# Optimization experiments

Hardware: AMD Instinct MI355X
Metric: run time of the kernel (lower is better)

The kernel has to match this reference:

```python
import jax, jax.numpy as jnp
import numpy as np

LDDT_THRESHOLDS = jnp.array([0.5, 1.0, 2.0, 4.0], dtype=jnp.float32)
NUCLEIC_ACID_CUTOFF = 30.0
OTHER_CUTOFF = 15.0


def _cdist(x):
    # pairwise euclidean distances, safe sqrt (zero grad on diagonal zeros)
    sq = jnp.sum(x * x, axis=-1)                      # [b, n]
    d2 = sq[:, :, None] + sq[:, None, :] - 2.0 * jnp.einsum('bic,bjc->bij', x, x)
    d2 = jnp.maximum(d2, 0.0)
    pos = d2 > 0.0
    return jnp.where(pos, jnp.sqrt(jnp.where(pos, d2, 1.0)), 0.0)


def setup_inputs() -> dict:
    key = jax.random.key(0)
    k1, k2, k3, k4, k5 = jax.random.split(key, 5)
    b, n = 2, 4096
    true_coords = jax.random.normal(k1, (b, n, 3), dtype=jnp.float32) * 10.0
    pred_coords = true_coords + jax.random.normal(k2, (b, n, 3), dtype=jnp.float32) * 1.0
    is_dna = jax.random.bernoulli(k3, 0.25, (b, n))
    is_rna = jax.random.bernoulli(k4, 0.25, (b, n))
    coords_mask = jax.random.bernoulli(k5, 0.9, (b, n))
    return {
        'pred_coords': pred_coords,
        'true_coords': true_coords,
        'is_dna': is_dna,
        'is_rna': is_rna,
        'coords_mask': coords_mask,
    }


def reference(pred_coords, true_coords, is_dna, is_rna, coords_mask):
    b, n, _ = pred_coords.shape
    pred_dists = _cdist(pred_coords)                  # [b, n, n]
    true_dists = _cdist(true_coords)                  # [b, n, n]
    dist_diff = jnp.abs(true_dists - pred_dists)      # [b, n, n]

    # sigmoid(threshold - dist_diff), averaged over the 4 thresholds
    eps = jax.nn.sigmoid(LDDT_THRESHOLDS - dist_diff[..., None]).mean(axis=-1)  # [b, n, n]

    is_nucleotide = is_dna | is_rna                   # [b, n]
    nuc_pair = is_nucleotide[:, :, None] & is_nucleotide[:, None, :]
    inclusion_radius = jnp.where(nuc_pair,
                                 true_dists < NUCLEIC_ACID_CUTOFF,
                                 true_dists < OTHER_CUTOFF)
    mask = inclusion_radius & ~jnp.eye(n, dtype=bool)[None]
    paired_coords_mask = coords_mask[:, :, None] & coords_mask[:, None, :]
    mask = mask & paired_coords_mask

    maskf = mask.astype(eps.dtype)
    num = jnp.sum(eps * maskf, axis=(-1, -2))         # [b]
    den = jnp.maximum(jnp.sum(maskf, axis=(-1, -2)), 1.0)
    lddt = num / den
    return 1.0 - lddt.mean()
```

## Files before the change

kernel.cpp:

```cpp
#include <hip/hip_runtime.h>
#include <math.h>

#define N      4096
#define BLOCK  256
#define JW     32
#define NITILE (N / BLOCK)
#define NTRI   1088
#define NQ     (JW / 4)

typedef float v4f __attribute__((ext_vector_type(4)));

#define PN0 4.0f
#define PN1 3.384183069f
#define PN2 0.750655861f
#define PN3 0.036699475f
#define PD1 1.128061023f
#define PD2 0.375327930f
#define PD3 0.036699475f
#define PD4 0.000553084f

__device__ __forceinline__ int tri_off(int t) { return 132 * t - 4 * t * t; }
__device__ __forceinline__ v4f splat(float x) { return (v4f){x, x, x, x}; }

__global__ __launch_bounds__(BLOCK, 4) void lddt_main_kernel(
    const float* __restrict__ pred, const float* __restrict__ truec,
    const int* __restrict__ is_dna, const int* __restrict__ is_rna,
    const int* __restrict__ cmask, float* __restrict__ ws)
{
    const int L     = blockIdx.x;
    const int batch = blockIdx.z;
    const int tid   = threadIdx.x;

    int itile = 0;
#pragma unroll
    for (int u = 1; u < NITILE; ++u) itile += (L >= tri_off(u)) ? 1 : 0;
    const int jseg = 8 * itile + (L - tri_off(itile));
    const bool diag = (jseg < 8 * itile + 8);

    const int i = itile * BLOCK + tid;

    const float* pb = pred  + (size_t)batch * N * 3;
    const float* tb = truec + (size_t)batch * N * 3;
    const int* dnab = is_dna + (size_t)batch * N;
    const int* rnab = is_rna + (size_t)batch * N;
    const int* cmb  = cmask  + (size_t)batch * N;

    __shared__ v4f spx[NQ], spy[NQ], spz[NQ], snw[NQ];
    __shared__ v4f stx[NQ], sty[NQ], stz[NQ], scw[NQ];
    const int j0 = jseg * JW;
    if (tid < JW) {
        const int j = j0 + tid;
        ((float*)spx)[tid] = pb[j*3+0];
        ((float*)spy)[tid] = pb[j*3+1];
        ((float*)spz)[tid] = pb[j*3+2];
        ((float*)snw)[tid] = (dnab[j] | rnab[j]) ? 675.0f : 0.0f;
        ((float*)stx)[tid] = tb[j*3+0];
        ((float*)sty)[tid] = tb[j*3+1];
        ((float*)stz)[tid] = tb[j*3+2];
        ((float*)scw)[tid] = cmb[j] ? 1.0f : 0.0f;
    }
    __syncthreads();

    const float pix = pb[i*3+0], piy = pb[i*3+1], piz = pb[i*3+2];
    const float tix = tb[i*3+0], tiy = tb[i*3+1], tiz = tb[i*3+2];
    const float inuc01 = (dnab[i] | rnab[i]) ? 1.0f : 0.0f;
    const float icm    = cmb[i] ? 1.0f : 0.0f;

    const v4f pix4 = splat(pix), piy4 = splat(piy), piz4 = splat(piz);
    const v4f tix4 = splat(tix), tiy4 = splat(tiy), tiz4 = splat(tiz);
    const v4f base = splat(225.0f);
    const v4f inuc4 = splat(inuc01);

    float num = 0.0f;
    v4f den4 = splat(0.0f);

#define PAIR4(Q, NEED_TRI)                                                     \
    {                                                                          \
        const v4f Px = spx[Q], Py = spy[Q], Pz = spz[Q], Pw = snw[Q];          \
        const v4f Tx = stx[Q], Ty = sty[Q], Tz = stz[Q], Tw = scw[Q];          \
        v4f dxp = pix4 - Px, dyp = piy4 - Py, dzp = piz4 - Pz;                 \
        v4f d2p = dxp * dxp + dyp * dyp + dzp * dzp;                           \
        v4f dxt = tix4 - Tx, dyt = tiy4 - Ty, dzt = tiz4 - Tz;                 \
        v4f d2t = dxt * dxt + dyt * dyt + dzt * dzt;                           \
        v4f dp, dt;                                                            \
        dp.x = __builtin_amdgcn_sqrtf(d2p.x); dt.x = __builtin_amdgcn_sqrtf(d2t.x); \
        dp.y = __builtin_amdgcn_sqrtf(d2p.y); dt.y = __builtin_amdgcn_sqrtf(d2t.y); \
        dp.z = __builtin_amdgcn_sqrtf(d2p.z); dt.z = __builtin_amdgcn_sqrtf(d2t.z); \
        dp.w = __builtin_amdgcn_sqrtf(d2p.w); dt.w = __builtin_amdgcn_sqrtf(d2t.w); \
        v4f dd = dt - dp;                                                      \
        v4f e;                                                                 \
        e.x = __expf(fminf(fabsf(dd.x), 10.0f));                               \
        e.y = __expf(fminf(fabsf(dd.y), 10.0f));                               \
        e.z = __expf(fminf(fabsf(dd.z), 10.0f));                               \
        e.w = __expf(fminf(fabsf(dd.w), 10.0f));                               \
        v4f NN = ((e * splat(PN3) + splat(PN2)) * e + splat(PN1)) * e + splat(PN0); \
        v4f ND = (((e * splat(PD4) + splat(PD3)) * e + splat(PD2)) * e + splat(PD1)) * e + splat(1.0f); \
        v4f cut = base + inuc4 * Pw;                                           \
        v4f m;                                                                 \
        { bool k0 = d2t.x < cut.x, k1 = d2t.y < cut.y,                         \
           k2 = d2t.z < cut.z, k3 = d2t.w < cut.w;                             \
          if (NEED_TRI) { const int jb = j0 + 4 * (Q);                         \
            k0 = k0 && (jb + 0 > i); k1 = k1 && (jb + 1 > i);                  \
            k2 = k2 && (jb + 2 > i); k3 = k3 && (jb + 3 > i); }                \
          m.x = k0 ? Tw.x : 0.0f; m.y = k1 ? Tw.y : 0.0f;                      \
          m.z = k2 ? Tw.z : 0.0f; m.w = k3 ? Tw.w : 0.0f; }                    \
        v4f t = m * NN;                                                        \
        den4 += m;                                                             \
        float na = fmaf(t.x, ND.y, t.y * ND.x);                                \
        num = fmaf(na, __builtin_amdgcn_rcpf(ND.x * ND.y), num);               \
        float nb = fmaf(t.z, ND.w, t.w * ND.z);                                \
        num = fmaf(nb, __builtin_amdgcn_rcpf(ND.z * ND.w), num);               \
    }

    if (diag) {
#pragma unroll 2
        for (int q = 0; q < NQ; ++q) PAIR4(q, true)
    } else {
#pragma unroll 2
        for (int q = 0; q < NQ; ++q) PAIR4(q, false)
    }
#undef PAIR4

    float den = den4.x + den4.y + den4.z + den4.w;

    num *= 0.5f * icm;
    den *= 2.0f * icm;

    for (int off = 32; off > 0; off >>= 1) {
        num += __shfl_down(num, off);
        den += __shfl_down(den, off);
    }
    __shared__ float rn[BLOCK / 64], rd[BLOCK / 64];
    const int wid = tid >> 6, lane = tid & 63;
    if (lane == 0) { rn[wid] = num; rd[wid] = den; }
    __syncthreads();
    if (tid == 0) {
        float tn = rn[0] + rn[1] + rn[2] + rn[3];
        float td = rd[0] + rd[1] + rd[2] + rd[3];
        const int bid = batch * NTRI + L;
        ws[bid * 2 + 0] = tn;
        ws[bid * 2 + 1] = td;
    }
}

__global__ __launch_bounds__(BLOCK) void finalize_kernel(
    const float* __restrict__ ws, float* __restrict__ out, int b)
{
    __shared__ float sn[4], sd[4];
    float acc = 0.0f;
    for (int k = 0; k < b; ++k) {
        float n = 0.0f, d = 0.0f;
        for (int p = threadIdx.x; p < NTRI; p += BLOCK) {
            n += ws[(k * NTRI + p) * 2 + 0];
            d += ws[(k * NTRI + p) * 2 + 1];
        }
        for (int off = 32; off > 0; off >>= 1) {
            n += __shfl_down(n, off);
            d += __shfl_down(d, off);
        }
        if ((threadIdx.x & 63) == 0) { sn[threadIdx.x >> 6] = n; sd[threadIdx.x >> 6] = d; }
        __syncthreads();
        if (threadIdx.x == 0) {
            float tn = sn[0] + sn[1] + sn[2] + sn[3];
            float td = sd[0] + sd[1] + sd[2] + sd[3];
            acc += tn / fmaxf(td, 1.0f);
        }
        __syncthreads();
    }
    if (threadIdx.x == 0) out[0] = 1.0f - acc / (float)b;
}

extern "C" void kernel_launch(void* const* d_in, const int* in_sizes, int n_in,
                              void* d_out, int out_size, void* d_ws, size_t ws_size,
                              hipStream_t stream) {
    const float* pred  = (const float*)d_in[0];
    const float* truec = (const float*)d_in[1];
    const int* is_dna  = (const int*)d_in[2];
    const int* is_rna  = (const int*)d_in[3];
    const int* cmask   = (const int*)d_in[4];
    float* out = (float*)d_out;
    float* ws  = (float*)d_ws;

    const int b = in_sizes[2] / N;

    dim3 grid(NTRI, 1, b);
    lddt_main_kernel<<<grid, BLOCK, 0, stream>>>(pred, truec, is_dna, is_rna, cmask, ws);
    finalize_kernel<<<1, BLOCK, 0, stream>>>(ws, out, b);
}
```

Baseline: 82.50 us.

## Shrink blocks to one wavefront with finer triangular tiling and merged reciprocal

Blocks shrink from 256 to 64 threads, each covering a 64-row i-tile against a 32-column j-segment. The triangular grid grows to 4160 blocks per batch, and the tile index is found with a sqrt-based closed form. Because each block is a single wavefront, the shared-memory cross-wave reduction and its barrier are dropped, and the pred and true coordinate loads into shared memory are split across both halves of the wave. Two other local changes fold the per-quad reciprocal into one rcp over four denominators and lower the exp clamp from 10 to 5, which slightly changes sigmoid tail accuracy for large distance errors.

Result: slower. 88.57 us (+7.4%).

```diff
diff --git a/kernel.cpp b/kernel.cpp
--- a/kernel.cpp
+++ b/kernel.cpp
@@ -2,11 +2,11 @@
 #include <math.h>
 
 #define N      4096
-#define BLOCK  256
+#define BLOCK  64
+#define IT     64
 #define JW     32
-#define NITILE (N / BLOCK)
-#define NTRI   1088
 #define NQ     (JW / 4)
+#define NTRI   4160
 
 typedef float v4f __attribute__((ext_vector_type(4)));
 
@@ -19,7 +19,6 @@
 #define PD3 0.036699475f
 #define PD4 0.000553084f
 
-__device__ __forceinline__ int tri_off(int t) { return 132 * t - 4 * t * t; }
 __device__ __forceinline__ v4f splat(float x) { return (v4f){x, x, x, x}; }
 
 __global__ __launch_bounds__(BLOCK, 4) void lddt_main_kernel(
@@ -31,13 +30,15 @@
     const int batch = blockIdx.z;
     const int tid   = threadIdx.x;
 
-    int itile = 0;
-#pragma unroll
-    for (int u = 1; u < NITILE; ++u) itile += (L >= tri_off(u)) ? 1 : 0;
-    const int jseg = 8 * itile + (L - tri_off(itile));
-    const bool diag = (jseg < 8 * itile + 8);
+    int t = (int)((129.0f - __builtin_amdgcn_sqrtf((float)(16641 - 4 * L))) * 0.5f);
+    t = (t > 63) ? 63 : ((t < 0) ? 0 : t);
+    while (t * (129 - t) > L) --t;
+    while ((t + 1) * (128 - t) <= L) ++t;
+    const int jloc = L - t * (129 - t);
+    const int j0   = 64 * t + 32 * jloc;
+    const bool diag = (jloc < 2);
 
-    const int i = itile * BLOCK + tid;
+    const int i = 64 * t + tid;
 
     const float* pb = pred  + (size_t)batch * N * 3;
     const float* tb = truec + (size_t)batch * N * 3;
@@ -47,17 +48,18 @@
 
     __shared__ v4f spx[NQ], spy[NQ], spz[NQ], snw[NQ];
     __shared__ v4f stx[NQ], sty[NQ], stz[NQ], scw[NQ];
-    const int j0 = jseg * JW;
     if (tid < JW) {
         const int j = j0 + tid;
         ((float*)spx)[tid] = pb[j*3+0];
         ((float*)spy)[tid] = pb[j*3+1];
         ((float*)spz)[tid] = pb[j*3+2];
         ((float*)snw)[tid] = (dnab[j] | rnab[j]) ? 675.0f : 0.0f;
-        ((float*)stx)[tid] = tb[j*3+0];
-        ((float*)sty)[tid] = tb[j*3+1];
-        ((float*)stz)[tid] = tb[j*3+2];
-        ((float*)scw)[tid] = cmb[j] ? 1.0f : 0.0f;
+    } else {
+        const int j = j0 + tid - JW;
+        ((float*)stx)[tid - JW] = tb[j*3+0];
+        ((float*)sty)[tid - JW] = tb[j*3+1];
+        ((float*)stz)[tid - JW] = tb[j*3+2];
+        ((float*)scw)[tid - JW] = cmb[j] ? 1.0f : 0.0f;
     }
     __syncthreads();
 
@@ -89,10 +91,10 @@
         dp.w = __builtin_amdgcn_sqrtf(d2p.w); dt.w = __builtin_amdgcn_sqrtf(d2t.w); \
         v4f dd = dt - dp;                                                      \
         v4f e;                                                                 \
-        e.x = __expf(fminf(fabsf(dd.x), 10.0f));                               \
-        e.y = __expf(fminf(fabsf(dd.y), 10.0f));                               \
-        e.z = __expf(fminf(fabsf(dd.z), 10.0f));                               \
-        e.w = __expf(fminf(fabsf(dd.w), 10.0f));                               \
+        e.x = __expf(fminf(fabsf(dd.x), 5.0f));                                \
+        e.y = __expf(fminf(fabsf(dd.y), 5.0f));                                \
+        e.z = __expf(fminf(fabsf(dd.z), 5.0f));                                \
+        e.w = __expf(fminf(fabsf(dd.w), 5.0f));                                \
         v4f NN = ((e * splat(PN3) + splat(PN2)) * e + splat(PN1)) * e + splat(PN0); \
         v4f ND = (((e * splat(PD4) + splat(PD3)) * e + splat(PD2)) * e + splat(PD1)) * e + splat(1.0f); \
         v4f cut = base + inuc4 * Pw;                                           \
@@ -104,12 +106,13 @@
             k2 = k2 && (jb + 2 > i); k3 = k3 && (jb + 3 > i); }                \
           m.x = k0 ? Tw.x : 0.0f; m.y = k1 ? Tw.y : 0.0f;                      \
           m.z = k2 ? Tw.z : 0.0f; m.w = k3 ? Tw.w : 0.0f; }                    \
-        v4f t = m * NN;                                                        \
+        v4f tt = m * NN;                                                       \
         den4 += m;                                                             \
-        float na = fmaf(t.x, ND.y, t.y * ND.x);                                \
-        num = fmaf(na, __builtin_amdgcn_rcpf(ND.x * ND.y), num);               \
-        float nb = fmaf(t.z, ND.w, t.w * ND.z);                                \
-        num = fmaf(nb, __builtin_amdgcn_rcpf(ND.z * ND.w), num);               \
+        float d12 = ND.x * ND.y, d34 = ND.z * ND.w;                            \
+        float a = fmaf(tt.x, ND.y, tt.y * ND.x);                               \
+        float c = fmaf(tt.z, ND.w, tt.w * ND.z);                               \
+        float nr = fmaf(a, d34, c * d12);                                      \
+        num = fmaf(nr, __builtin_amdgcn_rcpf(d12 * d34), num);                 \
     }
 
     if (diag) {
@@ -130,27 +133,21 @@
         num += __shfl_down(num, off);
         den += __shfl_down(den, off);
     }
-    __shared__ float rn[BLOCK / 64], rd[BLOCK / 64];
-    const int wid = tid >> 6, lane = tid & 63;
-    if (lane == 0) { rn[wid] = num; rd[wid] = den; }
-    __syncthreads();
     if (tid == 0) {
-        float tn = rn[0] + rn[1] + rn[2] + rn[3];
-        float td = rd[0] + rd[1] + rd[2] + rd[3];
         const int bid = batch * NTRI + L;
-        ws[bid * 2 + 0] = tn;
-        ws[bid * 2 + 1] = td;
+        ws[bid * 2 + 0] = num;
+        ws[bid * 2 + 1] = den;
     }
 }
 
-__global__ __launch_bounds__(BLOCK) void finalize_kernel(
+__global__ __launch_bounds__(256) void finalize_kernel(
     const float* __restrict__ ws, float* __restrict__ out, int b)
 {
     __shared__ float sn[4], sd[4];
     float acc = 0.0f;
     for (int k = 0; k < b; ++k) {
         float n = 0.0f, d = 0.0f;
-        for (int p = threadIdx.x; p < NTRI; p += BLOCK) {
+        for (int p = threadIdx.x; p < NTRI; p += 256) {
             n += ws[(k * NTRI + p) * 2 + 0];
             d += ws[(k * NTRI + p) * 2 + 1];
         }
@@ -185,5 +182,5 @@
 
     dim3 grid(NTRI, 1, b);
     lddt_main_kernel<<<grid, BLOCK, 0, stream>>>(pred, truec, is_dna, is_rna, cmask, ws);
-    finalize_kernel<<<1, BLOCK, 0, stream>>>(ws, out, b);
+    finalize_kernel<<<1, 256, 0, stream>>>(ws, out, b);
 }
```

## Pack pred/true coordinates in fp16 with log2e prescale and exp2 sigmoid

Applied to the files above, without the earlier changes.

Stores j-tile coordinates as interleaved half-precision pred/true pairs prescaled by log2(e). Squared distances are then computed with packed fp16 vector math, and exp2 replaces exp. The coords mask is folded into the true coordinates as a poison value that fails the cutoff test, and the two reciprocals per quad merge into one. This removes ALU work and shared-memory traffic, but fp16 distance arithmetic on coordinates around ±40 loses a lot of precision and can overflow. That risks large errors against the fp32 reference.

Result: slower. 85.11 us (+3.2%).

```diff
diff --git a/kernel.cpp b/kernel.cpp
--- a/kernel.cpp
+++ b/kernel.cpp
@@ -9,6 +9,14 @@
 #define NQ     (JW / 4)
 
 typedef float v4f __attribute__((ext_vector_type(4)));
+typedef _Float16 h2  __attribute__((ext_vector_type(2)));
+typedef _Float16 v8h __attribute__((ext_vector_type(8)));
+
+#define LOG2E   1.4426950408889634f
+#define BASE_SQ 468.30802f
+#define NUC_SQ  1404.92406f
+#define CLAMP_S 7.2134752f
+#define TPOISON ((_Float16)30000.0f)
 
 #define PN0 4.0f
 #define PN1 3.384183069f
@@ -45,30 +53,41 @@
     const int* rnab = is_rna + (size_t)batch * N;
     const int* cmb  = cmask  + (size_t)batch * N;
 
-    __shared__ v4f spx[NQ], spy[NQ], spz[NQ], snw[NQ];
-    __shared__ v4f stx[NQ], sty[NQ], stz[NQ], scw[NQ];
+    __shared__ v8h sx[NQ], sy[NQ], sz[NQ];
+    __shared__ v4f snw[NQ];
     const int j0 = jseg * JW;
     if (tid < JW) {
         const int j = j0 + tid;
-        ((float*)spx)[tid] = pb[j*3+0];
-        ((float*)spy)[tid] = pb[j*3+1];
-        ((float*)spz)[tid] = pb[j*3+2];
-        ((float*)snw)[tid] = (dnab[j] | rnab[j]) ? 675.0f : 0.0f;
-        ((float*)stx)[tid] = tb[j*3+0];
-        ((float*)sty)[tid] = tb[j*3+1];
-        ((float*)stz)[tid] = tb[j*3+2];
-        ((float*)scw)[tid] = cmb[j] ? 1.0f : 0.0f;
+        const bool jc = cmb[j] != 0;
+        h2 cx, cy, cz;
+        cx[0] = (_Float16)(pb[j*3+0] * LOG2E);
+        cy[0] = (_Float16)(pb[j*3+1] * LOG2E);
+        cz[0] = (_Float16)(pb[j*3+2] * LOG2E);
+        cx[1] = jc ? (_Float16)(tb[j*3+0] * LOG2E) : TPOISON;
+        cy[1] = jc ? (_Float16)(tb[j*3+1] * LOG2E) : TPOISON;
+        cz[1] = jc ? (_Float16)(tb[j*3+2] * LOG2E) : TPOISON;
+        ((h2*)sx)[tid] = cx;
+        ((h2*)sy)[tid] = cy;
+        ((h2*)sz)[tid] = cz;
+    } else if (tid < 2 * JW) {
+        const int j = j0 + tid - JW;
+        ((float*)snw)[tid - JW] = (dnab[j] | rnab[j]) ? NUC_SQ : 0.0f;
     }
     __syncthreads();
 
-    const float pix = pb[i*3+0], piy = pb[i*3+1], piz = pb[i*3+2];
-    const float tix = tb[i*3+0], tiy = tb[i*3+1], tiz = tb[i*3+2];
+    const float pix = pb[i*3+0] * LOG2E, piy = pb[i*3+1] * LOG2E, piz = pb[i*3+2] * LOG2E;
+    const float tix = tb[i*3+0] * LOG2E, tiy = tb[i*3+1] * LOG2E, tiz = tb[i*3+2] * LOG2E;
     const float inuc01 = (dnab[i] | rnab[i]) ? 1.0f : 0.0f;
     const float icm    = cmb[i] ? 1.0f : 0.0f;
 
-    const v4f pix4 = splat(pix), piy4 = splat(piy), piz4 = splat(piz);
-    const v4f tix4 = splat(tix), tiy4 = splat(tiy), tiz4 = splat(tiz);
-    const v4f base = splat(225.0f);
+    const h2 ix2 = {(_Float16)pix, (_Float16)tix};
+    const h2 iy2 = {(_Float16)piy, (_Float16)tiy};
+    const h2 iz2 = {(_Float16)piz, (_Float16)tiz};
+    const v8h ix8 = {ix2[0], ix2[1], ix2[0], ix2[1], ix2[0], ix2[1], ix2[0], ix2[1]};
+    const v8h iy8 = {iy2[0], iy2[1], iy2[0], iy2[1], iy2[0], iy2[1], iy2[0], iy2[1]};
+    const v8h iz8 = {iz2[0], iz2[1], iz2[0], iz2[1], iz2[0], iz2[1], iz2[0], iz2[1]};
+
+    const v4f base  = splat(BASE_SQ);
     const v4f inuc4 = splat(inuc01);
 
     float num = 0.0f;
@@ -76,40 +95,39 @@
 
 #define PAIR4(Q, NEED_TRI)                                                     \
     {                                                                          \
-        const v4f Px = spx[Q], Py = spy[Q], Pz = spz[Q], Pw = snw[Q];          \
-        const v4f Tx = stx[Q], Ty = sty[Q], Tz = stz[Q], Tw = scw[Q];          \
-        v4f dxp = pix4 - Px, dyp = piy4 - Py, dzp = piz4 - Pz;                 \
-        v4f d2p = dxp * dxp + dyp * dyp + dzp * dzp;                           \
-        v4f dxt = tix4 - Tx, dyt = tiy4 - Ty, dzt = tiz4 - Tz;                 \
-        v4f d2t = dxt * dxt + dyt * dyt + dzt * dzt;                           \
+        v8h dx = ix8 - sx[Q], dy = iy8 - sy[Q], dz = iz8 - sz[Q];              \
+        v8h d2 = dx * dx + dy * dy + dz * dz;      \
+        v4f d2p4 = {(float)d2[0], (float)d2[2], (float)d2[4], (float)d2[6]};   \
+        v4f d2t4 = {(float)d2[1], (float)d2[3], (float)d2[5], (float)d2[7]};   \
         v4f dp, dt;                                                            \
-        dp.x = __builtin_amdgcn_sqrtf(d2p.x); dt.x = __builtin_amdgcn_sqrtf(d2t.x); \
-        dp.y = __builtin_amdgcn_sqrtf(d2p.y); dt.y = __builtin_amdgcn_sqrtf(d2t.y); \
-        dp.z = __builtin_amdgcn_sqrtf(d2p.z); dt.z = __builtin_amdgcn_sqrtf(d2t.z); \
-        dp.w = __builtin_amdgcn_sqrtf(d2p.w); dt.w = __builtin_amdgcn_sqrtf(d2t.w); \
+        dp.x = __builtin_amdgcn_sqrtf(d2p4.x); dt.x = __builtin_amdgcn_sqrtf(d2t4.x); \
+        dp.y = __builtin_amdgcn_sqrtf(d2p4.y); dt.y = __builtin_amdgcn_sqrtf(d2t4.y); \
+        dp.z = __builtin_amdgcn_sqrtf(d2p4.z); dt.z = __builtin_amdgcn_sqrtf(d2t4.z); \
+        dp.w = __builtin_amdgcn_sqrtf(d2p4.w); dt.w = __builtin_amdgcn_sqrtf(d2t4.w); \
         v4f dd = dt - dp;                                                      \
-        v4f e;                                                                 \
-        e.x = __expf(fminf(fabsf(dd.x), 10.0f));                               \
-        e.y = __expf(fminf(fabsf(dd.y), 10.0f));                               \
-        e.z = __expf(fminf(fabsf(dd.z), 10.0f));                               \
-        e.w = __expf(fminf(fabsf(dd.w), 10.0f));                               \
+        v4f e;                       \
+        e.x = __builtin_amdgcn_exp2f(fminf(fabsf(dd.x), CLAMP_S));             \
+        e.y = __builtin_amdgcn_exp2f(fminf(fabsf(dd.y), CLAMP_S));             \
+        e.z = __builtin_amdgcn_exp2f(fminf(fabsf(dd.z), CLAMP_S));             \
+        e.w = __builtin_amdgcn_exp2f(fminf(fabsf(dd.w), CLAMP_S));             \
         v4f NN = ((e * splat(PN3) + splat(PN2)) * e + splat(PN1)) * e + splat(PN0); \
         v4f ND = (((e * splat(PD4) + splat(PD3)) * e + splat(PD2)) * e + splat(PD1)) * e + splat(1.0f); \
-        v4f cut = base + inuc4 * Pw;                                           \
+        v4f cut = base + inuc4 * snw[Q];                                       \
         v4f m;                                                                 \
-        { bool k0 = d2t.x < cut.x, k1 = d2t.y < cut.y,                         \
-           k2 = d2t.z < cut.z, k3 = d2t.w < cut.w;                             \
+        { bool k0 = d2t4.x < cut.x, k1 = d2t4.y < cut.y,                       \
+           k2 = d2t4.z < cut.z, k3 = d2t4.w < cut.w;                           \
           if (NEED_TRI) { const int jb = j0 + 4 * (Q);                         \
             k0 = k0 && (jb + 0 > i); k1 = k1 && (jb + 1 > i);                  \
             k2 = k2 && (jb + 2 > i); k3 = k3 && (jb + 3 > i); }                \
-          m.x = k0 ? Tw.x : 0.0f; m.y = k1 ? Tw.y : 0.0f;                      \
-          m.z = k2 ? Tw.z : 0.0f; m.w = k3 ? Tw.w : 0.0f; }                    \
-        v4f t = m * NN;                                                        \
+          m.x = k0 ? 1.0f : 0.0f; m.y = k1 ? 1.0f : 0.0f;                      \
+          m.z = k2 ? 1.0f : 0.0f; m.w = k3 ? 1.0f : 0.0f; }                    \
+        v4f tt = m * NN;                                                       \
         den4 += m;                                                             \
-        float na = fmaf(t.x, ND.y, t.y * ND.x);                                \
-        num = fmaf(na, __builtin_amdgcn_rcpf(ND.x * ND.y), num);               \
-        float nb = fmaf(t.z, ND.w, t.w * ND.z);                                \
-        num = fmaf(nb, __builtin_amdgcn_rcpf(ND.z * ND.w), num);               \
+        float d12 = ND.x * ND.y, d34 = ND.z * ND.w;                            \
+        float a = fmaf(tt.x, ND.y, tt.y * ND.x);                               \
+        float c = fmaf(tt.z, ND.w, tt.w * ND.z);                               \
+        float nr = fmaf(a, d34, c * d12);                                      \
+        num = fmaf(nr, __builtin_amdgcn_rcpf(d12 * d34), num);                 \
     }
 
     if (diag) {
```
